# Performance work log

Measured on AMD Instinct MI355X. Metric: run time of the kernel, lower is better.

The kernel has to match this reference:

```python
import jax, jax.numpy as jnp
import numpy as np

N_NODES = 100_000
N_EDGES = 1_600_000
F_IN = 128
HID = 64
C_OUT = 16


def setup_inputs() -> dict:
    key = jax.random.key(0)
    k1, k2, k3, k4, k5 = jax.random.split(key, 5)
    x = jax.random.normal(k1, (N_NODES, F_IN), dtype=jnp.float32)
    edge_index = jax.random.randint(k2, (2, N_EDGES), 0, N_NODES, dtype=jnp.int64)
    edge_weight = jax.random.uniform(k3, (N_EDGES,), dtype=jnp.float32)
    # Glorot-ish init for the two GCNConv linear layers; PyG inits bias to zero.
    W1 = jax.random.normal(k4, (F_IN, HID), dtype=jnp.float32) * (1.0 / np.sqrt(F_IN))
    b1 = jnp.zeros((HID,), dtype=jnp.float32)
    W2 = jax.random.normal(k5, (HID, C_OUT), dtype=jnp.float32) * (1.0 / np.sqrt(HID))
    b2 = jnp.zeros((C_OUT,), dtype=jnp.float32)
    return {"x": x, "edge_index": edge_index, "edge_weight": edge_weight,
            "W1": W1, "b1": b1, "W2": W2, "b2": b2}


def gcn_layer(x, row, col, ew, W, b, n):
    """PyG GCNConv: h = D^-1/2 (A + I) D^-1/2 (x W) + b, with edge weights.
    Self loops (weight 1) are handled analytically instead of appending edges."""
    h = x @ W  # [n, out]
    deg = jax.ops.segment_sum(ew, col, num_segments=n) + 1.0  # +1 for self loop
    dinv = jax.lax.rsqrt(deg)  # deg >= 1 always
    norm = dinv[row] * ew * dinv[col]  # [E]
    agg = jax.ops.segment_sum(norm[:, None] * h[row], col, num_segments=n)
    return agg + (dinv * dinv)[:, None] * h + b


def reference(x, edge_index, edge_weight, W1, b1, W2, b2):
    row, col = edge_index[0], edge_index[1]
    h = jax.nn.relu(gcn_layer(x, row, col, edge_weight, W1, b1, N_NODES))
    # delete_min_weighted_edges(node=0): remove the min-weight edge with source 0.
    # Zeroing its weight is mathematically identical to deleting it (it then
    # contributes 0 to both the degree and the aggregation).
    masked = jnp.where(row == 0, edge_weight, jnp.inf)
    idx = jnp.argmin(masked)
    ew2 = edge_weight.at[idx].set(0.0)
    return gcn_layer(h, row, col, ew2, W2, b2, N_NODES)
```

## Files before the change

### kernel.cpp

```cpp
#include <hip/hip_runtime.h>
#include <hip/hip_bf16.h>
#include <stdint.h>

#define NN 100000
#define NE 1600000
#define FIN 128
#define HID 64
#define COUT 16

#define BUKSH 8
#define BUKN 256
#define NBUK ((NN + BUKN - 1) >> BUKSH)
#define CAP 5120
#define PART_NB 200
#define EPB (NE / PART_NB)

typedef unsigned long long u64;
typedef short bf16x8 __attribute__((ext_vector_type(8)));
typedef float f32x4 __attribute__((ext_vector_type(4)));

struct Flags { int f32; int i64; };

__device__ __forceinline__ float b2f(__hip_bfloat16 v) { return __bfloat162float(v); }

__device__ __forceinline__ float ldf(const void* p, size_t i, int f32) {
    return f32 ? ((const float*)p)[i]
               : __bfloat162float(((const __hip_bfloat16*)p)[i]);
}
__device__ __forceinline__ int lde(const void* p, size_t i, int i64) {
    return i64 ? (int)((const long long*)p)[i] : ((const int*)p)[i];
}
__device__ __forceinline__ void ld4bf(const __hip_bfloat16* p, float& x0, float& x1,
                                      float& x2, float& x3) {
    union { uint2 u; __hip_bfloat16 h[4]; } v;
    v.u = *(const uint2*)p;
    x0 = b2f(v.h[0]); x1 = b2f(v.h[1]); x2 = b2f(v.h[2]); x3 = b2f(v.h[3]);
}
__device__ __forceinline__ unsigned short f2bfu(float f) {
    union { __hip_bfloat16 b; unsigned short u; } c;
    c.b = __float2bfloat16(f);
    return c.u;
}
__device__ __forceinline__ float bfu2f(unsigned short u) {
    union { unsigned short h[2]; float f; } c;
    c.h[0] = 0; c.h[1] = u;
    return c.f;
}

__global__ __launch_bounds__(256) void k_init(const unsigned short* xs,
                                              const int* ei32, Flags* fl,
                                              int* cursorA, u64* minkey,
                                              int* delpos) {
    int t = threadIdx.x;
    if (t < 64) {
        int lane = t;
        int huge = 0;
        for (int i = lane * 2; i < 1024; i += 128) {
            int e = (xs[i] >> 7) & 0xFF;
            if (e >= 0xC0) huge = 1;
        }
        int odd_nonzero = 0;
        for (int i = 1 + lane * 2; i < 512; i += 128) {
            if (ei32[i] != 0) odd_nonzero = 1;
        }
        u64 h = __ballot(huge), o = __ballot(odd_nonzero);
        if (lane == 0) { fl->f32 = (h != 0); fl->i64 = (o == 0); }
    }
    for (int i = t; i < NBUK; i += 256) cursorA[i] = 0;
    if (t == 64) *minkey = ~0ull;
    if (t == 65) *delpos = 0x7fffffff;
}

__global__ void k_mink(const void* __restrict__ ei, const void* __restrict__ ew,
                       const Flags* __restrict__ fl, u64* __restrict__ minkey) {
    int e = blockIdx.x * blockDim.x + threadIdx.x;
    if (e >= NE) return;
    int r = lde(ei, e, fl->i64);
    if (r == 0) {
        float w = ldf(ew, e, fl->f32);
        u64 key = ((u64)__float_as_uint(w) << 32) | (unsigned)e;
        atomicMin(minkey, key);
    }
}

__global__ __launch_bounds__(256) void k_partA(const void* __restrict__ ei,
                                               const void* __restrict__ ew,
                                               const Flags* __restrict__ fl,
                                               int* __restrict__ cursorA,
                                               long long* __restrict__ tmp) {
    __shared__ int cnt[NBUK];
    __shared__ int base[NBUK];
    int b = blockIdx.x, t = threadIdx.x;
    int f32 = fl->f32, i64 = fl->i64;
    for (int i = t; i < NBUK; i += 256) cnt[i] = 0;
    __syncthreads();
    int e0 = b * EPB;
    for (int i = t; i < EPB; i += 256) {
        int c = lde(ei, (size_t)NE + e0 + i, i64);
        atomicAdd(&cnt[c >> BUKSH], 1);
    }
    __syncthreads();
    for (int i = t; i < NBUK; i += 256) {
        int n = cnt[i];
        base[i] = n ? atomicAdd(&cursorA[i], n) : 0;
    }
    __syncthreads();
    for (int i = t; i < NBUK; i += 256) cnt[i] = 0;
    __syncthreads();
    for (int i = t; i < EPB; i += 256) {
        int e = e0 + i;
        int r = lde(ei, e, i64);
        int c = lde(ei, (size_t)NE + e, i64);
        float w = ldf(ew, e, f32);
        int buk = c >> BUKSH;
        int slot = base[buk] + atomicAdd(&cnt[buk], 1);
        if (slot < CAP) {
            unsigned lo = (unsigned)r | (((unsigned)c & 255u) << 17);
            tmp[(size_t)buk * CAP + slot] = ((long long)__float_as_int(w) << 32) | lo;
        }
    }
}

__global__ __launch_bounds__(256) void k_partB(const int* __restrict__ cursorA,
                                               const long long* __restrict__ tmp,
                                               int2* __restrict__ epack,
                                               int* __restrict__ rowptrN,
                                               const void* __restrict__ ei,
                                               const void* __restrict__ ew,
                                               const Flags* __restrict__ fl,
                                               const u64* __restrict__ minkey,
                                               float* __restrict__ dinv1,
                                               float* __restrict__ dinv2,
                                               int* __restrict__ delpos) {
    __shared__ int cnt[256];
    __shared__ int pfx[256];
    __shared__ u64 wsum[256];
    int b = blockIdx.x, t = threadIdx.x;
    int partial = 0;
    for (int i = t; i < NBUK; i += 256) {
        int cc = cursorA[i]; if (cc > CAP) cc = CAP;
        if (i < b) partial += cc;
    }
    pfx[t] = partial;
    __syncthreads();
    for (int off = 128; off > 0; off >>= 1) {
        if (t < off) pfx[t] += pfx[t + off];
        __syncthreads();
    }
    int gbase = pfx[0];
    __syncthreads();
    cnt[t] = 0; wsum[t] = 0;
    __syncthreads();
    int count = cursorA[b]; if (count > CAP) count = CAP;
    if (b == NBUK - 1 && t == 0) rowptrN[NN] = gbase + count;
    u64 kk = *minkey;
    int eidx = (kk == ~0ull) ? 0 : (int)(kk & 0xffffffffu);
    int smin  = lde(ei, (size_t)eidx, fl->i64);
    int cmin  = lde(ei, (size_t)NE + eidx, fl->i64);
    int wminb = __float_as_int(ldf(ew, eidx, fl->f32));
    bool myb = (b == (cmin >> BUKSH));
    int clow = cmin & 255;
    const long long* ts = tmp + (size_t)b * CAP;
    for (int i = t; i < count; i += 256) {
        long long pk = ts[i];
        unsigned lo = (unsigned)pk;
        int nl = (int)((lo >> 17) & 255u);
        atomicAdd(&cnt[nl], 1);
        float w = __int_as_float((int)(pk >> 32));
        atomicAdd(&wsum[nl], (u64)((double)w * 4294967296.0));
    }
    __syncthreads();
    int v = cnt[t];
    pfx[t] = v;
    for (int off = 1; off < 256; off <<= 1) {
        __syncthreads();
        int add = (t >= off) ? pfx[t - off] : 0;
        __syncthreads();
        pfx[t] += add;
    }
    __syncthreads();
    int excl = pfx[t] - v;
    int node = (b << BUKSH) + t;
    if (node < NN) {
        rowptrN[node] = gbase + excl;
        float degv = (float)((double)wsum[t] * (1.0 / 4294967296.0));
        float d1 = degv + 1.0f;
        float d2 = d1 - ((node == cmin) ? __int_as_float(wminb) : 0.0f);
        dinv1[node] = rsqrtf(d1);
        dinv2[node] = rsqrtf(d2);
    }
    __syncthreads();
    cnt[t] = gbase + excl;
    __syncthreads();
    for (int i = t; i < count; i += 256) {
        long long pk = ts[i];
        unsigned lo = (unsigned)pk;
        int nl = (int)((lo >> 17) & 255u);
        int pos = atomicAdd(&cnt[nl], 1);
        long long outpk = (pk & 0xFFFFFFFF00000000LL) | (lo & 0x1FFFFu);
        *(long long*)(epack + pos) = outpk;
        if (myb && nl == clow && (int)(lo & 0x1FFFFu) == smin
            && (int)(pk >> 32) == wminb)
            atomicMin(delpos, pos);
    }
}

__global__ __launch_bounds__(256, 3) void k_gemm1(const void* __restrict__ xv_,
                                                  const void* __restrict__ W1_,
                                                  const Flags* __restrict__ fl,
                                                  const float* __restrict__ dinv1,
                                                  __hip_bfloat16* __restrict__ h1) {
    __shared__ __align__(16) unsigned short Wbuf[16384];
    int t = threadIdx.x;
    int wave = t >> 6, lane = t & 63;
    int quad = lane >> 4, col = lane & 15;
    if (fl->f32) {
        const float* x  = (const float*)xv_;
        const float* W1 = (const float*)W1_;
        unsigned short* Whi = Wbuf;
        unsigned short* Wlo = Wbuf + 8192;
        for (int i = t; i < 8192; i += 256) {
            int k = i >> 6;
            int n = i & 63;
            int kc = k >> 5, kr = k & 31;
            int q = kr >> 3, j = kr & 7;
            int n0 = n >> 4, c2 = n & 15;
            float w = W1[i];
            unsigned short hi = f2bfu(w);
            unsigned short lo = f2bfu(w - bfu2f(hi));
            int idx = ((n0 << 4) + (kc << 2) + q) * 128 + c2 * 8 + j;
            Whi[idx] = hi;
            Wlo[idx] = lo;
        }
        __syncthreads();
        bf16x8 Bh[4][4];
#pragma unroll
        for (int n0 = 0; n0 < 4; ++n0)
#pragma unroll
            for (int kc = 0; kc < 4; ++kc)
                Bh[kc][n0] = *(const bf16x8*)&Whi[((n0 << 4) + (kc << 2) + quad) * 128 + col * 8];
        int tile0 = (blockIdx.x * 4 + wave) * 2;
#pragma unroll 1
        for (int i = 0; i < 2; ++i) {
            int node0 = (tile0 + i) * 16;
            if (node0 >= NN) return;
            const float* xp = x + (size_t)(node0 + col) * FIN + quad * 8;
            float4 xv[8];
#pragma unroll
            for (int kc = 0; kc < 4; ++kc) {
                xv[2 * kc]     = *(const float4*)(xp + kc * 32);
                xv[2 * kc + 1] = *(const float4*)(xp + kc * 32 + 4);
            }
            f32x4 a0 = {0.f, 0.f, 0.f, 0.f}, a1 = a0, a2 = a0, a3 = a0;
#pragma unroll
            for (int kc = 0; kc < 4; ++kc) {
                float fv[8];
                fv[0] = xv[2 * kc].x;     fv[1] = xv[2 * kc].y;
                fv[2] = xv[2 * kc].z;     fv[3] = xv[2 * kc].w;
                fv[4] = xv[2 * kc + 1].x; fv[5] = xv[2 * kc + 1].y;
                fv[6] = xv[2 * kc + 1].z; fv[7] = xv[2 * kc + 1].w;
                bf16x8 Ah, Al;
#pragma unroll
                for (int j = 0; j < 8; ++j) {
                    unsigned short hi = f2bfu(fv[j]);
                    Ah[j] = (short)hi;
                    Al[j] = (short)f2bfu(fv[j] - bfu2f(hi));
                }
                int lbase = ((kc << 2) + quad) * 128 + col * 8;
                bf16x8 Bl0 = *(const bf16x8*)&Wlo[lbase];
                bf16x8 Bl1 = *(const bf16x8*)&Wlo[(1 << 4) * 128 + lbase];
                bf16x8 Bl2 = *(const bf16x8*)&Wlo[(2 << 4) * 128 + lbase];
                bf16x8 Bl3 = *(const bf16x8*)&Wlo[(3 << 4) * 128 + lbase];
                a0 = __builtin_amdgcn_mfma_f32_16x16x32_bf16(Ah, Bh[kc][0], a0, 0, 0, 0);
                a0 = __builtin_amdgcn_mfma_f32_16x16x32_bf16(Al, Bh[kc][0], a0, 0, 0, 0);
                a0 = __builtin_amdgcn_mfma_f32_16x16x32_bf16(Ah, Bl0,      a0, 0, 0, 0);
                a1 = __builtin_amdgcn_mfma_f32_16x16x32_bf16(Ah, Bh[kc][1], a1, 0, 0, 0);
                a1 = __builtin_amdgcn_mfma_f32_16x16x32_bf16(Al, Bh[kc][1], a1, 0, 0, 0);
                a1 = __builtin_amdgcn_mfma_f32_16x16x32_bf16(Ah, Bl1,      a1, 0, 0, 0);
                a2 = __builtin_amdgcn_mfma_f32_16x16x32_bf16(Ah, Bh[kc][2], a2, 0, 0, 0);
                a2 = __builtin_amdgcn_mfma_f32_16x16x32_bf16(Al, Bh[kc][2], a2, 0, 0, 0);
                a2 = __builtin_amdgcn_mfma_f32_16x16x32_bf16(Ah, Bl2,      a2, 0, 0, 0);
                a3 = __builtin_amdgcn_mfma_f32_16x16x32_bf16(Ah, Bh[kc][3], a3, 0, 0, 0);
                a3 = __builtin_amdgcn_mfma_f32_16x16x32_bf16(Al, Bh[kc][3], a3, 0, 0, 0);
                a3 = __builtin_amdgcn_mfma_f32_16x16x32_bf16(Ah, Bl3,      a3, 0, 0, 0);
            }
            __hip_bfloat16* hp = h1 + (size_t)(node0 + quad * 4) * HID + col;
#pragma unroll
            for (int r = 0; r < 4; ++r) {
                float dsc = dinv1[node0 + quad * 4 + r];
                hp[(size_t)r * HID + 0]  = __float2bfloat16(a0[r] * dsc);
                hp[(size_t)r * HID + 16] = __float2bfloat16(a1[r] * dsc);
                hp[(size_t)r * HID + 32] = __float2bfloat16(a2[r] * dsc);
                hp[(size_t)r * HID + 48] = __float2bfloat16(a3[r] * dsc);
            }
        }
    } else {
        const __hip_bfloat16* x = (const __hip_bfloat16*)xv_;
        const unsigned short* W1 = (const unsigned short*)W1_;
        unsigned short* Wf = Wbuf;
        for (int i = t; i < 8192; i += 256) {
            int k = i >> 6;
            int n = i & 63;
            int kc = k >> 5, kr = k & 31;
            int q = kr >> 3, j = kr & 7;
            int n0 = n >> 4, c2 = n & 15;
            Wf[((((n0 << 2) | kc) << 2) | q) * 128 + c2 * 8 + j] = W1[i];
        }
        __syncthreads();
        bf16x8 B[4][4];
#pragma unroll
        for (int n0 = 0; n0 < 4; ++n0)
#pragma unroll
            for (int kc = 0; kc < 4; ++kc)
                B[kc][n0] = *(const bf16x8*)&Wf[((((n0 << 2) | kc) << 2) | quad) * 128 + col * 8];
        int tile0 = (blockIdx.x * 4 + wave) * 2;
#pragma unroll 1
        for (int i = 0; i < 2; ++i) {
            int node0 = (tile0 + i) * 16;
            if (node0 >= NN) return;
            const __hip_bfloat16* xp = x + (size_t)(node0 + col) * FIN + quad * 8;
            f32x4 a0 = {0.f, 0.f, 0.f, 0.f}, a1 = a0, a2 = a0, a3 = a0;
#pragma unroll
            for (int kc = 0; kc < 4; ++kc) {
                bf16x8 A = *(const bf16x8*)(xp + kc * 32);
                a0 = __builtin_amdgcn_mfma_f32_16x16x32_bf16(A, B[kc][0], a0, 0, 0, 0);
                a1 = __builtin_amdgcn_mfma_f32_16x16x32_bf16(A, B[kc][1], a1, 0, 0, 0);
                a2 = __builtin_amdgcn_mfma_f32_16x16x32_bf16(A, B[kc][2], a2, 0, 0, 0);
                a3 = __builtin_amdgcn_mfma_f32_16x16x32_bf16(A, B[kc][3], a3, 0, 0, 0);
            }
            __hip_bfloat16* hp = h1 + (size_t)(node0 + quad * 4) * HID + col;
#pragma unroll
            for (int r = 0; r < 4; ++r) {
                float dsc = dinv1[node0 + quad * 4 + r];
                hp[(size_t)r * HID + 0]  = __float2bfloat16(a0[r] * dsc);
                hp[(size_t)r * HID + 16] = __float2bfloat16(a1[r] * dsc);
                hp[(size_t)r * HID + 32] = __float2bfloat16(a2[r] * dsc);
                hp[(size_t)r * HID + 48] = __float2bfloat16(a3[r] * dsc);
            }
        }
    }
}

__global__ __launch_bounds__(256) void k_agg1(const int* __restrict__ rowptrN,
                                              const int2* __restrict__ epack,
                                              const float* __restrict__ dinv1,
                                              const __hip_bfloat16* __restrict__ h1,
                                              const void* __restrict__ b1,
                                              const void* __restrict__ W2,
                                              const Flags* __restrict__ fl,
                                              const float* __restrict__ dinv2,
                                              float* __restrict__ h2) {
    __shared__ float Ws[HID * COUT];
    __shared__ float obuf[16][68];
    int t = threadIdx.x;
    int f32 = fl->f32;
    for (int i = t; i < HID * COUT; i += 256) Ws[i] = ldf(W2, i, f32);
    int nn = t >> 4;
    int n = blockIdx.x * 16 + nn;
    int l = t & 15;
    int f = l * 4;
    int wbase = t & 48;
    float dn = dinv1[n];
    int p0 = rowptrN[n], p1 = rowptrN[n + 1];
    float a0 = 0.f, a1 = 0.f, a2 = 0.f, a3 = 0.f;
    for (int p = p0; p < p1; p += 16) {
        int idx = p + l;
        int2 ev = make_int2(0, 0);
        if (idx < p1) ev = epack[idx];
        float cw = __int_as_float(ev.y);
        int rj[16];
#pragma unroll
        for (int j = 0; j < 16; ++j)
            rj[j] = __shfl(ev.x, wbase + j);
        uint2 raw[16];
#pragma unroll
        for (int j = 0; j < 16; ++j)
            raw[j] = *(const uint2*)(h1 + (size_t)rj[j] * HID + f);
#pragma unroll
        for (int j = 0; j < 16; ++j) {
            float c = __shfl(cw, wbase + j);
            union { uint2 u; __hip_bfloat16 h[4]; } v; v.u = raw[j];
            a0 += c * b2f(v.h[0]);
            a1 += c * b2f(v.h[1]);
            a2 += c * b2f(v.h[2]);
            a3 += c * b2f(v.h[3]);
        }
    }
    float x0, x1, x2, x3;
    ld4bf(h1 + (size_t)n * HID + f, x0, x1, x2, x3);
    obuf[nn][f + 0] = fmaxf(dn * (a0 + x0) + ldf(b1, f + 0, f32), 0.f);
    obuf[nn][f + 1] = fmaxf(dn * (a1 + x1) + ldf(b1, f + 1, f32), 0.f);
    obuf[nn][f + 2] = fmaxf(dn * (a2 + x2) + ldf(b1, f + 2, f32), 0.f);
    obuf[nn][f + 3] = fmaxf(dn * (a3 + x3) + ldf(b1, f + 3, f32), 0.f);
    __syncthreads();
    int c = t & 15;
    const float* orow = obuf[nn];
    float acc = 0.f;
#pragma unroll 8
    for (int k = 0; k < HID; ++k)
        acc += orow[k] * Ws[k * COUT + c];
    h2[(size_t)n * COUT + c] = acc * dinv2[n];
}

__global__ __launch_bounds__(256) void k_agg2(const int* __restrict__ rowptrN,
                                              const int2* __restrict__ epack,
                                              const float* __restrict__ dinv2,
                                              const float* __restrict__ h2,
                                              const void* __restrict__ bias2,
                                              const Flags* __restrict__ fl,
                                              const int* __restrict__ delpos,
                                              void* __restrict__ out) {
    int t = threadIdx.x;
    int n = blockIdx.x * 64 + (t >> 2);
    if (n >= NN) return;
    int l = t & 3;
    int f = l * 4;
    int wbase = t & 60;
    int f32 = fl->f32;
    int dp = *delpos;
    float dn = dinv2[n];
    int p0 = rowptrN[n], p1 = rowptrN[n + 1];
    float a0 = 0.f, a1 = 0.f, a2 = 0.f, a3 = 0.f;
    for (int p = p0; p < p1; p += 8) {
        int iA = p + l, iB = p + 4 + l;
        int2 evA = make_int2(0, 0), evB = make_int2(0, 0);
        if (iA < p1) evA = epack[iA];
        if (iB < p1) evB = epack[iB];
        float cwA = (iA == dp) ? 0.f : __int_as_float(evA.y);
        float cwB = (iB == dp) ? 0.f : __int_as_float(evB.y);
        int rj[8];
#pragma unroll
        for (int j = 0; j < 4; ++j) {
            rj[j]     = __shfl(evA.x, wbase + j);
            rj[4 + j] = __shfl(evB.x, wbase + j);
        }
        float4 hv[8];
#pragma unroll
        for (int j = 0; j < 8; ++j)
            hv[j] = *(const float4*)(h2 + (size_t)rj[j] * COUT + f);
#pragma unroll
        for (int j = 0; j < 4; ++j) {
            float cA = __shfl(cwA, wbase + j);
            float cB = __shfl(cwB, wbase + j);
            a0 += cA * hv[j].x + cB * hv[4 + j].x;
            a1 += cA * hv[j].y + cB * hv[4 + j].y;
            a2 += cA * hv[j].z + cB * hv[4 + j].z;
            a3 += cA * hv[j].w + cB * hv[4 + j].w;
        }
    }
    const float4 hn = *(const float4*)(h2 + (size_t)n * COUT + f);
    float o0 = dn * (a0 + hn.x) + ldf(bias2, f + 0, f32);
    float o1 = dn * (a1 + hn.y) + ldf(bias2, f + 1, f32);
    float o2 = dn * (a2 + hn.z) + ldf(bias2, f + 2, f32);
    float o3 = dn * (a3 + hn.w) + ldf(bias2, f + 3, f32);
    size_t idx = (size_t)n * COUT + f;
    if (f32) {
        float* op = (float*)out + idx;
        op[0] = o0; op[1] = o1; op[2] = o2; op[3] = o3;
    } else {
        union { uint2 u; __hip_bfloat16 h[4]; } pk;
        pk.h[0] = __float2bfloat16(o0); pk.h[1] = __float2bfloat16(o1);
        pk.h[2] = __float2bfloat16(o2); pk.h[3] = __float2bfloat16(o3);
        *(uint2*)((__hip_bfloat16*)out + idx) = pk.u;
    }
}

extern "C" void kernel_launch(void* const* d_in, const int* in_sizes, int n_in,
                              void* d_out, int out_size, void* d_ws, size_t ws_size,
                              hipStream_t stream) {
    const void* x  = d_in[0];
    const void* ei = d_in[1];
    const void* ew = d_in[2];
    const void* W1 = d_in[3];
    const void* b1 = d_in[4];
    const void* W2 = d_in[5];
    const void* b2 = d_in[6];

    char* wsb = (char*)d_ws;
    float* dinv1    = (float*)wsb;                     wsb += (size_t)NN * 4;
    float* dinv2    = (float*)wsb;                     wsb += (size_t)NN * 4;
    int*   rowptrN  = (int*)wsb;                       wsb += (size_t)(NN + 1) * 4;
    int*   cursorA  = (int*)wsb;                       wsb += (size_t)NBUK * 4;
    wsb = (char*)(((uintptr_t)wsb + 15) & ~(uintptr_t)15);
    int2*  epack    = (int2*)wsb;                      wsb += (size_t)NE * 8;
    __hip_bfloat16* h1 = (__hip_bfloat16*)wsb;         wsb += (size_t)NN * HID * 2;
    float* h2       = (float*)wsb;                     wsb += (size_t)NN * COUT * 4;
    long long* tmp  = (long long*)wsb;                 wsb += (size_t)NBUK * CAP * 8;
    u64*   minkey   = (u64*)wsb;                       wsb += 8;
    Flags* fl       = (Flags*)wsb;                     wsb += 8;
    int*   delpos   = (int*)wsb;                       wsb += 8;

    k_init<<<1, 256, 0, stream>>>((const unsigned short*)x, (const int*)ei, fl,
                                  cursorA, minkey, delpos);
    k_mink<<<(NE + 255) / 256, 256, 0, stream>>>(ei, ew, fl, minkey);
    k_partA<<<PART_NB, 256, 0, stream>>>(ei, ew, fl, cursorA, tmp);
    k_partB<<<NBUK, 256, 0, stream>>>(cursorA, tmp, epack, rowptrN,
                                      ei, ew, fl, minkey, dinv1, dinv2, delpos);
    k_gemm1<<<(NN / 16 + 7) / 8, 256, 0, stream>>>(x, W1, fl, dinv1, h1);
    k_agg1<<<NN / 16, 256, 0, stream>>>(rowptrN, epack, dinv1, h1, b1, W2, fl,
                                        dinv2, h2);
    k_agg2<<<(NN + 63) / 64, 256, 0, stream>>>(rowptrN, epack, dinv2, h2, b2, fl,
                                               delpos, d_out);
}
```

Baseline: 260.6 us.

## Replace capped-bucket partition with exact histogram-scan-scatter counting sort

The edge bucketing moves from a capped per-bucket staging buffer filled through global atomic cursors to a deterministic counting sort: per-block histograms, a two-kernel scan producing exact per-block bucket offsets, and a scatter into a dense temporary array. The min-weight search is folded into the histogram pass, which removes a separate full pass over the edges. The second partition kernel stages each bucket's edges in shared memory so its two passes avoid a second global read. The pipeline gains two extra launches and reads the edge indices twice, but drops the capacity truncation and the cross-block atomics.

```diff
diff --git a/kernel.cpp b/kernel.cpp
--- a/kernel.cpp
+++ b/kernel.cpp
@@ -9,11 +9,10 @@
 #define COUT 16
 
 #define BUKSH 8
-#define BUKN 256
-#define NBUK ((NN + BUKN - 1) >> BUKSH)
-#define CAP 5120
-#define PART_NB 200
+#define NBUK ((NN + 255) >> BUKSH)
+#define PART_NB 512
 #define EPB (NE / PART_NB)
+#define TSLCAP 5632
 
 typedef unsigned long long u64;
 typedef short bf16x8 __attribute__((ext_vector_type(8)));
@@ -47,81 +46,127 @@
     return c.f;
 }
 
-__global__ __launch_bounds__(256) void k_init(const unsigned short* xs,
-                                              const int* ei32, Flags* fl,
-                                              int* cursorA, u64* minkey,
-                                              int* delpos) {
-    int t = threadIdx.x;
-    if (t < 64) {
-        int lane = t;
-        int huge = 0;
-        for (int i = lane * 2; i < 1024; i += 128) {
-            int e = (xs[i] >> 7) & 0xFF;
-            if (e >= 0xC0) huge = 1;
-        }
-        int odd_nonzero = 0;
-        for (int i = 1 + lane * 2; i < 512; i += 128) {
-            if (ei32[i] != 0) odd_nonzero = 1;
-        }
-        u64 h = __ballot(huge), o = __ballot(odd_nonzero);
-        if (lane == 0) { fl->f32 = (h != 0); fl->i64 = (o == 0); }
-    }
-    for (int i = t; i < NBUK; i += 256) cursorA[i] = 0;
-    if (t == 64) *minkey = ~0ull;
-    if (t == 65) *delpos = 0x7fffffff;
-}
-
-__global__ void k_mink(const void* __restrict__ ei, const void* __restrict__ ew,
-                       const Flags* __restrict__ fl, u64* __restrict__ minkey) {
-    int e = blockIdx.x * blockDim.x + threadIdx.x;
-    if (e >= NE) return;
-    int r = lde(ei, e, fl->i64);
-    if (r == 0) {
-        float w = ldf(ew, e, fl->f32);
-        u64 key = ((u64)__float_as_uint(w) << 32) | (unsigned)e;
-        atomicMin(minkey, key);
-    }
-}
-
-__global__ __launch_bounds__(256) void k_partA(const void* __restrict__ ei,
-                                               const void* __restrict__ ew,
-                                               const Flags* __restrict__ fl,
-                                               int* __restrict__ cursorA,
-                                               long long* __restrict__ tmp) {
+__global__ __launch_bounds__(64) void k_init(const unsigned short* xs,
+                                             const int* ei32, Flags* fl,
+                                             u64* minkey, int* delpos,
+                                             int* rowptrN) {
+    int lane = threadIdx.x;
+    int huge = 0;
+    for (int i = lane * 2; i < 1024; i += 128) {
+        int e = (xs[i] >> 7) & 0xFF;
+        if (e >= 0xC0) huge = 1;
+    }
+    int odd_nonzero = 0;
+    for (int i = 1 + lane * 2; i < 512; i += 128) {
+        if (ei32[i] != 0) odd_nonzero = 1;
+    }
+    u64 h = __ballot(huge), o = __ballot(odd_nonzero);
+    if (lane == 0) {
+        fl->f32 = (h != 0); fl->i64 = (o == 0);
+        *minkey = ~0ull;
+        *delpos = 0x7fffffff;
+        rowptrN[NN] = NE;
+    }
+}
+
+__global__ __launch_bounds__(512) void k_hist(const void* __restrict__ ei,
+                                              const void* __restrict__ ew,
+                                              const Flags* __restrict__ fl,
+                                              int* __restrict__ blockhist,
+                                              u64* __restrict__ minkey) {
     __shared__ int cnt[NBUK];
-    __shared__ int base[NBUK];
     int b = blockIdx.x, t = threadIdx.x;
     int f32 = fl->f32, i64 = fl->i64;
-    for (int i = t; i < NBUK; i += 256) cnt[i] = 0;
+    for (int i = t; i < NBUK; i += 512) cnt[i] = 0;
     __syncthreads();
     int e0 = b * EPB;
-    for (int i = t; i < EPB; i += 256) {
-        int c = lde(ei, (size_t)NE + e0 + i, i64);
+    for (int i = t; i < EPB; i += 512) {
+        int e = e0 + i;
+        int c = lde(ei, (size_t)NE + e, i64);
         atomicAdd(&cnt[c >> BUKSH], 1);
-    }
-    __syncthreads();
-    for (int i = t; i < NBUK; i += 256) {
-        int n = cnt[i];
-        base[i] = n ? atomicAdd(&cursorA[i], n) : 0;
-    }
-    __syncthreads();
-    for (int i = t; i < NBUK; i += 256) cnt[i] = 0;
-    __syncthreads();
-    for (int i = t; i < EPB; i += 256) {
+        int r = lde(ei, (size_t)e, i64);
+        if (r == 0) {
+            float w = ldf(ew, e, f32);
+            u64 key = ((u64)__float_as_uint(w) << 32) | (unsigned)e;
+            atomicMin(minkey, key);
+        }
+    }
+    __syncthreads();
+    for (int i = t; i < NBUK; i += 512)
+        blockhist[(size_t)b * NBUK + i] = cnt[i];
+}
+
+__global__ __launch_bounds__(256) void k_scan1(const int* __restrict__ blockhist,
+                                               int* __restrict__ buktotal) {
+    __shared__ int sm[256];
+    int i = blockIdx.x, t = threadIdx.x;
+    int s = 0;
+    for (int b = t; b < PART_NB; b += 256) s += blockhist[(size_t)b * NBUK + i];
+    sm[t] = s;
+    __syncthreads();
+    for (int off = 128; off > 0; off >>= 1) {
+        if (t < off) sm[t] += sm[t + off];
+        __syncthreads();
+    }
+    if (t == 0) buktotal[i] = sm[0];
+}
+
+__global__ __launch_bounds__(512) void k_scan2(const int* __restrict__ blockhist,
+                                               const int* __restrict__ buktotal,
+                                               int* __restrict__ blockbase,
+                                               int* __restrict__ bucketBaseArr) {
+    __shared__ int pfx[512];
+    __shared__ int bbs;
+    int i = blockIdx.x, t = threadIdx.x;
+    pfx[t] = (t < i && t < NBUK) ? buktotal[t] : 0;
+    __syncthreads();
+    for (int off = 256; off > 0; off >>= 1) {
+        if (t < off) pfx[t] += pfx[t + off];
+        __syncthreads();
+    }
+    if (t == 0) { bbs = pfx[0]; bucketBaseArr[i] = pfx[0]; }
+    __syncthreads();
+    int gbase = bbs;
+    __syncthreads();
+    int v = blockhist[(size_t)t * NBUK + i];
+    pfx[t] = v;
+    for (int off = 1; off < 512; off <<= 1) {
+        __syncthreads();
+        int add = (t >= off) ? pfx[t - off] : 0;
+        __syncthreads();
+        pfx[t] += add;
+    }
+    __syncthreads();
+    blockbase[(size_t)t * NBUK + i] = gbase + pfx[t] - v;
+}
+
+__global__ __launch_bounds__(512) void k_scat(const void* __restrict__ ei,
+                                              const void* __restrict__ ew,
+                                              const Flags* __restrict__ fl,
+                                              const int* __restrict__ blockbase,
+                                              long long* __restrict__ tmp) {
+    __shared__ int cnt[NBUK];
+    int b = blockIdx.x, t = threadIdx.x;
+    int f32 = fl->f32, i64 = fl->i64;
+    for (int i = t; i < NBUK; i += 512) cnt[i] = 0;
+    __syncthreads();
+    int e0 = b * EPB;
+    const int* bb = blockbase + (size_t)b * NBUK;
+    for (int i = t; i < EPB; i += 512) {
         int e = e0 + i;
-        int r = lde(ei, e, i64);
         int c = lde(ei, (size_t)NE + e, i64);
+        int r = lde(ei, (size_t)e, i64);
         float w = ldf(ew, e, f32);
         int buk = c >> BUKSH;
-        int slot = base[buk] + atomicAdd(&cnt[buk], 1);
-        if (slot < CAP) {
-            unsigned lo = (unsigned)r | (((unsigned)c & 255u) << 17);
-            tmp[(size_t)buk * CAP + slot] = ((long long)__float_as_int(w) << 32) | lo;
-        }
-    }
-}
-
-__global__ __launch_bounds__(256) void k_partB(const int* __restrict__ cursorA,
+        int local = atomicAdd(&cnt[buk], 1);
+        int pos = bb[buk] + local;
+        unsigned lo = (unsigned)r | (((unsigned)c & 255u) << 17);
+        tmp[pos] = ((long long)__float_as_int(w) << 32) | lo;
+    }
+}
+
+__global__ __launch_bounds__(512) void k_partB(const int* __restrict__ buktotal,
+                                               const int* __restrict__ bucketBaseArr,
                                                const long long* __restrict__ tmp,
                                                int2* __restrict__ epack,
                                                int* __restrict__ rowptrN,
@@ -132,27 +177,36 @@
                                                float* __restrict__ dinv1,
                                                float* __restrict__ dinv2,
                                                int* __restrict__ delpos) {
+    __shared__ long long tsl[TSLCAP];
     __shared__ int cnt[256];
     __shared__ int pfx[256];
     __shared__ u64 wsum[256];
     int b = blockIdx.x, t = threadIdx.x;
-    int partial = 0;
-    for (int i = t; i < NBUK; i += 256) {
-        int cc = cursorA[i]; if (cc > CAP) cc = CAP;
-        if (i < b) partial += cc;
-    }
-    pfx[t] = partial;
-    __syncthreads();
-    for (int off = 128; off > 0; off >>= 1) {
-        if (t < off) pfx[t] += pfx[t + off];
-        __syncthreads();
-    }
-    int gbase = pfx[0];
-    __syncthreads();
-    cnt[t] = 0; wsum[t] = 0;
-    __syncthreads();
-    int count = cursorA[b]; if (count > CAP) count = CAP;
-    if (b == NBUK - 1 && t == 0) rowptrN[NN] = gbase + count;
+    int count = buktotal[b];
+    int gbase = bucketBaseArr[b];
+    const long long* ts = tmp + gbase;
+    int stage = count < TSLCAP ? count : TSLCAP;
+    for (int i = t; i < stage; i += 512) tsl[i] = ts[i];
+    if (t < 256) { cnt[t] = 0; wsum[t] = 0; }
+    __syncthreads();
+    for (int i = t; i < count; i += 512) {
+        long long pk = (i < TSLCAP) ? tsl[i] : ts[i];
+        unsigned lo = (unsigned)pk;
+        int nl = (int)((lo >> 17) & 255u);
+        atomicAdd(&cnt[nl], 1);
+        float w = __int_as_float((int)(pk >> 32));
+        atomicAdd(&wsum[nl], (u64)((double)w * 4294967296.0));
+    }
+    __syncthreads();
+    int v = 0;
+    if (t < 256) { v = cnt[t]; pfx[t] = v; }
+    for (int off = 1; off < 256; off <<= 1) {
+        __syncthreads();
+        int add = (t < 256 && t >= off) ? pfx[t - off] : 0;
+        __syncthreads();
+        if (t < 256) pfx[t] += add;
+    }
+    __syncthreads();
     u64 kk = *minkey;
     int eidx = (kk == ~0ull) ? 0 : (int)(kk & 0xffffffffu);
     int smin  = lde(ei, (size_t)eidx, fl->i64);
@@ -160,40 +214,22 @@
     int wminb = __float_as_int(ldf(ew, eidx, fl->f32));
     bool myb = (b == (cmin >> BUKSH));
     int clow = cmin & 255;
-    const long long* ts = tmp + (size_t)b * CAP;
-    for (int i = t; i < count; i += 256) {
-        long long pk = ts[i];
-        unsigned lo = (unsigned)pk;
-        int nl = (int)((lo >> 17) & 255u);
-        atomicAdd(&cnt[nl], 1);
-        float w = __int_as_float((int)(pk >> 32));
-        atomicAdd(&wsum[nl], (u64)((double)w * 4294967296.0));
-    }
-    __syncthreads();
-    int v = cnt[t];
-    pfx[t] = v;
-    for (int off = 1; off < 256; off <<= 1) {
-        __syncthreads();
-        int add = (t >= off) ? pfx[t - off] : 0;
-        __syncthreads();
-        pfx[t] += add;
-    }
-    __syncthreads();
-    int excl = pfx[t] - v;
-    int node = (b << BUKSH) + t;
-    if (node < NN) {
-        rowptrN[node] = gbase + excl;
-        float degv = (float)((double)wsum[t] * (1.0 / 4294967296.0));
-        float d1 = degv + 1.0f;
-        float d2 = d1 - ((node == cmin) ? __int_as_float(wminb) : 0.0f);
-        dinv1[node] = rsqrtf(d1);
-        dinv2[node] = rsqrtf(d2);
-    }
-    __syncthreads();
-    cnt[t] = gbase + excl;
-    __syncthreads();
-    for (int i = t; i < count; i += 256) {
-        long long pk = ts[i];
+    if (t < 256) {
+        int excl = pfx[t] - v;
+        int node = (b << BUKSH) + t;
+        if (node < NN) {
+            rowptrN[node] = gbase + excl;
+            float degv = (float)((double)wsum[t] * (1.0 / 4294967296.0));
+            float d1 = degv + 1.0f;
+            float d2 = d1 - ((node == cmin) ? __int_as_float(wminb) : 0.0f);
+            dinv1[node] = rsqrtf(d1);
+            dinv2[node] = rsqrtf(d2);
+        }
+        cnt[t] = gbase + excl;
+    }
+    __syncthreads();
+    for (int i = t; i < count; i += 512) {
+        long long pk = (i < TSLCAP) ? tsl[i] : ts[i];
         unsigned lo = (unsigned)pk;
         int nl = (int)((lo >> 17) & 255u);
         int pos = atomicAdd(&cnt[nl], 1);
@@ -477,24 +513,29 @@
     const void* b2 = d_in[6];
 
     char* wsb = (char*)d_ws;
+    int*   blockhist = (int*)wsb;                      wsb += (size_t)PART_NB * NBUK * 4;
+    int*   blockbase = (int*)wsb;                      wsb += (size_t)PART_NB * NBUK * 4;
+    int*   buktotal  = (int*)wsb;                      wsb += (size_t)NBUK * 4;
+    int*   bucketBaseArr = (int*)wsb;                  wsb += (size_t)NBUK * 4;
     float* dinv1    = (float*)wsb;                     wsb += (size_t)NN * 4;
     float* dinv2    = (float*)wsb;                     wsb += (size_t)NN * 4;
     int*   rowptrN  = (int*)wsb;                       wsb += (size_t)(NN + 1) * 4;
-    int*   cursorA  = (int*)wsb;                       wsb += (size_t)NBUK * 4;
     wsb = (char*)(((uintptr_t)wsb + 15) & ~(uintptr_t)15);
     int2*  epack    = (int2*)wsb;                      wsb += (size_t)NE * 8;
     __hip_bfloat16* h1 = (__hip_bfloat16*)wsb;         wsb += (size_t)NN * HID * 2;
     float* h2       = (float*)wsb;                     wsb += (size_t)NN * COUT * 4;
-    long long* tmp  = (long long*)wsb;                 wsb += (size_t)NBUK * CAP * 8;
+    long long* tmp  = (long long*)wsb;                 wsb += (size_t)NE * 8;
     u64*   minkey   = (u64*)wsb;                       wsb += 8;
     Flags* fl       = (Flags*)wsb;                     wsb += 8;
     int*   delpos   = (int*)wsb;                       wsb += 8;
 
-    k_init<<<1, 256, 0, stream>>>((const unsigned short*)x, (const int*)ei, fl,
-                                  cursorA, minkey, delpos);
-    k_mink<<<(NE + 255) / 256, 256, 0, stream>>>(ei, ew, fl, minkey);
-    k_partA<<<PART_NB, 256, 0, stream>>>(ei, ew, fl, cursorA, tmp);
-    k_partB<<<NBUK, 256, 0, stream>>>(cursorA, tmp, epack, rowptrN,
+    k_init<<<1, 64, 0, stream>>>((const unsigned short*)x, (const int*)ei, fl,
+                                 minkey, delpos, rowptrN);
+    k_hist<<<PART_NB, 512, 0, stream>>>(ei, ew, fl, blockhist, minkey);
+    k_scan1<<<NBUK, 256, 0, stream>>>(blockhist, buktotal);
+    k_scan2<<<NBUK, 512, 0, stream>>>(blockhist, buktotal, blockbase, bucketBaseArr);
+    k_scat<<<PART_NB, 512, 0, stream>>>(ei, ew, fl, blockbase, tmp);
+    k_partB<<<NBUK, 512, 0, stream>>>(buktotal, bucketBaseArr, tmp, epack, rowptrN,
                                       ei, ew, fl, minkey, dinv1, dinv2, delpos);
     k_gemm1<<<(NN / 16 + 7) / 8, 256, 0, stream>>>(x, W1, fl, dinv1, h1);
     k_agg1<<<NN / 16, 256, 0, stream>>>(rowptrN, epack, dinv1, h1, b1, W2, fl,
```

Result: faster. 245.8 us (-5.7%).
